# Performance work log

Measured on AMD Instinct MI355X. Metric: run time of the kernel, lower is better.

Reference implementation:

```python
import jax, jax.numpy as jnp
import numpy as np

EMBED_DIM = 768
FF_DIM = 3072
NUM_EXPERTS = 8
TOP_K = 2
CAPACITY_FACTOR = 1.25  # training-mode capacity factor
LB_WEIGHT = 0.01
Z_WEIGHT = 0.001


def setup_inputs() -> dict:
    key = jax.random.key(0)
    k0, k1, k2, k3, k4 = jax.random.split(key, 5)
    B, S, D, F, E = 4, 2048, EMBED_DIM, FF_DIM, NUM_EXPERTS
    scale_d = 1.0 / np.sqrt(D)
    scale_f = 1.0 / np.sqrt(F)
    return {
        "x": jax.random.normal(k0, (B, S, D), dtype=jnp.float32),
        # router gate: nn.Linear(D, E, bias=False) -> weight [E, D]
        "w_gate": jax.random.normal(k1, (E, D), dtype=jnp.float32) * scale_d,
        # stacked expert weights, torch Linear layout [out, in]
        "wi_gate": jax.random.normal(k2, (E, F, D), dtype=jnp.float32) * scale_d,
        "wi_up": jax.random.normal(k3, (E, F, D), dtype=jnp.float32) * scale_d,
        "wo": jax.random.normal(k4, (E, D, F), dtype=jnp.float32) * scale_f,
    }


def moe_forward(x, w_gate, wi_gate, wi_up, wo):
    B, S, D = x.shape
    E = w_gate.shape[0]
    K = TOP_K
    T = B * S
    capacity = max(int(T * K / E * CAPACITY_FACTOR), K)

    xf = x.reshape(T, D)
    router_logits = xf @ w_gate.T                        # [T, E]
    router_probs = jax.nn.softmax(router_logits, axis=-1)
    topk_probs, topk_idx = jax.lax.top_k(router_probs, K)  # [T, K]
    topk_probs = topk_probs / topk_probs.sum(axis=-1, keepdims=True)

    # one-hot dispatch mask [T, K, E]
    onehot = (topk_idx[:, :, None] == jnp.arange(E)[None, None, :]).astype(xf.dtype)
    # per-(k, expert) arrival rank of each token (torch truncates first `capacity`
    # tokens in token-index order, independently per k and per expert)
    rank = ((jnp.cumsum(onehot, axis=0) - onehot) * onehot).sum(-1)  # [T, K]
    keep = (rank < capacity).astype(xf.dtype)                        # [T, K]

    # combine weights per (token, expert) [T, E]
    combine = jnp.einsum('tk,tk,tke->te', topk_probs, keep, onehot)

    out = jnp.zeros_like(xf)
    for e in range(E):  # fixed small structural loop over experts
        gate = jax.nn.silu(xf @ wi_gate[e].T)   # [T, F]
        up = xf @ wi_up[e].T                    # [T, F]
        y = (gate * up) @ wo[e].T               # [T, D]
        out = out + y * combine[:, e:e + 1]

    # auxiliary losses
    expert_mask = onehot.sum(axis=1)            # [T, E]
    f = expert_mask.sum(axis=0) / (T * K)
    P = router_probs.mean(axis=0)
    load_balance_loss = E * (f * P).sum()
    z_loss = jnp.mean(jax.nn.logsumexp(router_logits, axis=-1) ** 2)
    aux_loss = LB_WEIGHT * load_balance_loss + Z_WEIGHT * z_loss

    return out.reshape(B, S, D), aux_loss


def reference(x, w_gate, wi_gate, wi_up, wo):
    return moe_forward(x, w_gate, wi_gate, wi_up, wo)
```

## Files before the change

kernel.cpp:

```cpp
#include <hip/hip_runtime.h>

typedef unsigned short u16;
typedef unsigned int u32;
typedef unsigned long long u64;

#define T_TOK 8192
#define DIM 768
#define FF 3072
#define NE 8
#define CAP 2560
#define LSTR 5120
#define MAXMT 20

typedef __attribute__((ext_vector_type(8))) short s8v;
typedef __attribute__((ext_vector_type(4))) float f4v;

__device__ __forceinline__ u16 f2bf(float f) {
  union { float f; u32 u; } v; v.f = f;
  u32 r = v.u + 0x7FFFu + ((v.u >> 16) & 1u);
  return (u16)(r >> 16);
}

__device__ __forceinline__ void glds16(const void* g, void* l) {
  __builtin_amdgcn_global_load_lds(
      (const __attribute__((address_space(1))) u32*)g,
      (__attribute__((address_space(3))) u32*)l, 16, 0, 0);
}

__global__ void cast_bf16_kernel(const float* __restrict__ src, u16* __restrict__ dst, int n8) {
  int i = blockIdx.x * blockDim.x + threadIdx.x;
  if (i >= n8) return;
  const float4* s4 = (const float4*)src;
  float4 a = s4[2 * i], b = s4[2 * i + 1];
  uint4 o;
  o.x = (u32)f2bf(a.x) | ((u32)f2bf(a.y) << 16);
  o.y = (u32)f2bf(a.z) | ((u32)f2bf(a.w) << 16);
  o.z = (u32)f2bf(b.x) | ((u32)f2bf(b.y) << 16);
  o.w = (u32)f2bf(b.z) | ((u32)f2bf(b.w) << 16);
  ((uint4*)dst)[i] = o;
}

__global__ __launch_bounds__(256) void router_kernel(
    const float* __restrict__ x, const float* __restrict__ wg,
    int* __restrict__ tki, float* __restrict__ tkp,
    float* __restrict__ probs, float* __restrict__ lse2) {
  int lane = threadIdx.x & 63;
  int t = blockIdx.x * 4 + (threadIdx.x >> 6);
  const float* xr = x + (long)t * DIM;
  float acc[NE];
#pragma unroll
  for (int e = 0; e < NE; e++) acc[e] = 0.f;
  for (int i = 0; i < DIM / 64; i++) {
    float xv = xr[lane + 64 * i];
#pragma unroll
    for (int e = 0; e < NE; e++) acc[e] += xv * wg[e * DIM + lane + 64 * i];
  }
#pragma unroll
  for (int off = 32; off > 0; off >>= 1) {
#pragma unroll
    for (int e = 0; e < NE; e++) acc[e] += __shfl_xor(acc[e], off);
  }
  if (lane == 0) {
    float m = acc[0];
#pragma unroll
    for (int e = 1; e < NE; e++) m = fmaxf(m, acc[e]);
    float p[NE], s = 0.f;
#pragma unroll
    for (int e = 0; e < NE; e++) { p[e] = __expf(acc[e] - m); s += p[e]; }
    float inv = 1.f / s;
    int e0 = 0;
#pragma unroll
    for (int e = 1; e < NE; e++) if (acc[e] > acc[e0]) e0 = e;
    int e1 = (e0 == 0) ? 1 : 0;
#pragma unroll
    for (int e = 0; e < NE; e++) if (e != e0 && acc[e] > acc[e1]) e1 = e;
    float p0 = p[e0] * inv, p1 = p[e1] * inv;
    float rn = 1.f / (p0 + p1);
    tki[2 * t] = e0; tki[2 * t + 1] = e1;
    tkp[2 * t] = p0 * rn; tkp[2 * t + 1] = p1 * rn;
    float4 pa = {p[0] * inv, p[1] * inv, p[2] * inv, p[3] * inv};
    float4 pb = {p[4] * inv, p[5] * inv, p[6] * inv, p[7] * inv};
    ((float4*)(probs + t * 8))[0] = pa;
    ((float4*)(probs + t * 8))[1] = pb;
    float lse = __logf(s) + m;
    lse2[t] = lse * lse;
  }
}

__global__ __launch_bounds__(1024) void reduce_router_kernel(
    const int* __restrict__ tki, const float* __restrict__ probs, const float* __restrict__ lse2,
    int* __restrict__ fcnt, float* __restrict__ psum, float* __restrict__ zsum) {
  int t = blockIdx.x * 1024 + threadIdx.x;
  float4 pa = ((const float4*)(probs + t * 8))[0];
  float4 pb = ((const float4*)(probs + t * 8))[1];
  float p[8] = {pa.x, pa.y, pa.z, pa.w, pb.x, pb.y, pb.z, pb.w};
  float z = lse2[t];
  int e0 = tki[2 * t], e1 = tki[2 * t + 1];
  int fc[8];
#pragma unroll
  for (int e = 0; e < 8; e++) fc[e] = (e0 == e ? 1 : 0) + (e1 == e ? 1 : 0);
#pragma unroll
  for (int off = 32; off > 0; off >>= 1) {
#pragma unroll
    for (int e = 0; e < 8; e++) { p[e] += __shfl_xor(p[e], off); fc[e] += __shfl_xor(fc[e], off); }
    z += __shfl_xor(z, off);
  }
  __shared__ float sp[16][9];
  __shared__ int sf[16][8];
  int wv = threadIdx.x >> 6, lane = threadIdx.x & 63;
  if (lane == 0) {
#pragma unroll
    for (int e = 0; e < 8; e++) { sp[wv][e] = p[e]; sf[wv][e] = fc[e]; }
    sp[wv][8] = z;
  }
  __syncthreads();
  if (threadIdx.x < 9) {
    float s = 0.f;
    for (int w = 0; w < 16; w++) s += sp[w][threadIdx.x];
    if (threadIdx.x < 8) atomicAdd(&psum[threadIdx.x], s);
    else atomicAdd(zsum, s);
  }
  if (threadIdx.x >= 64 && threadIdx.x < 72) {
    int e = threadIdx.x - 64;
    int s = 0;
    for (int w = 0; w < 16; w++) s += sf[w][e];
    atomicAdd(&fcnt[e], s);
  }
}

__global__ __launch_bounds__(1024) void rank_dispatch_kernel(
    const int* __restrict__ tki, const float* __restrict__ tkp,
    int* __restrict__ ltk, float* __restrict__ lw,
    int* __restrict__ counts, int* __restrict__ baserow) {
  __shared__ int wave_cnt[2][16][8];
  __shared__ int base[2][8];
  __shared__ int epos[8];
  int tid = threadIdx.x, wv = tid >> 6, lane = tid & 63;
  if (tid < 16) base[tid >> 3][tid & 7] = 0;
  if (tid < 8) epos[tid] = 0;
  __syncthreads();
  u64 lmask = (lane == 63) ? 0x7FFFFFFFFFFFFFFFull : ((1ull << lane) - 1ull);
  for (int c = 0; c < T_TOK / 1024; c++) {
    int t = c * 1024 + tid;
    int e0 = tki[2 * t], e1 = tki[2 * t + 1];
    float p0 = tkp[2 * t], p1 = tkp[2 * t + 1];
    int pre0 = 0, pre1 = 0;
    for (int e = 0; e < 8; e++) {
      u64 m0 = __ballot(e0 == e);
      if (e0 == e) pre0 = __popcll(m0 & lmask);
      if (lane == 0) wave_cnt[0][wv][e] = __popcll(m0);
      u64 m1 = __ballot(e1 == e);
      if (e1 == e) pre1 = __popcll(m1 & lmask);
      if (lane == 0) wave_cnt[1][wv][e] = __popcll(m1);
    }
    __syncthreads();
    if (tid < 16) {
      int k = tid >> 3, e = tid & 7;
      int run = base[k][e];
      for (int w = 0; w < 16; w++) {
        int v = wave_cnt[k][w][e];
        wave_cnt[k][w][e] = run;
        run += v;
      }
      base[k][e] = run;
    }
    __syncthreads();
    int r0 = wave_cnt[0][wv][e0] + pre0;
    int r1 = wave_cnt[1][wv][e1] + pre1;
    if (r0 < CAP) { int p = atomicAdd(&epos[e0], 1); ltk[e0 * LSTR + p] = (t << 1); lw[e0 * LSTR + p] = p0; }
    if (r1 < CAP) { int p = atomicAdd(&epos[e1], 1); ltk[e1 * LSTR + p] = (t << 1) | 1; lw[e1 * LSTR + p] = p1; }
    __syncthreads();
  }
  if (tid == 0) {
    int run = 0;
    for (int e = 0; e < 8; e++) { counts[e] = epos[e]; baserow[e] = run; run += epos[e]; }
  }
}

__global__ __launch_bounds__(256, 2) void gemm1_kernel(
    const u16* __restrict__ xb, const u16* __restrict__ wgb, const u16* __restrict__ wub,
    u16* __restrict__ H, const int* __restrict__ counts, const int* __restrict__ baserow,
    const int* __restrict__ ltk) {
  int id = blockIdx.x;
  int xcd = id & 7;
  int q = id >> 3;
  int gg = q / MAXMT;
  int mt = q - gg * MAXMT;
  int g = gg * 8 + xcd;
  int e = g / 48;
  int nt = g - e * 48;
  int cnt = counts[e];
  if (mt * 128 >= cnt) return;

  __shared__ u16 As[128 * 64];
  __shared__ u16 Bg[64 * 64];
  __shared__ u16 Bu[64 * 64];
  __shared__ int toks[128];
  int tid = threadIdx.x;
  if (tid < 128) {
    int r = mt * 128 + tid; if (r > cnt - 1) r = cnt - 1;
    toks[tid] = ltk[e * LSTR + r] >> 1;
  }
  __syncthreads();
  int rq8 = tid >> 3;
  int swz = ((tid & 7) ^ (rq8 & 7)) * 8;
  long tA0 = toks[rq8], tA1 = toks[32 + rq8], tA2 = toks[64 + rq8], tA3 = toks[96 + rq8];
  const u16* gA0 = xb + tA0 * DIM + swz;
  const u16* gA1 = xb + tA1 * DIM + swz;
  const u16* gA2 = xb + tA2 * DIM + swz;
  const u16* gA3 = xb + tA3 * DIM + swz;
  long bO0 = ((long)e * FF + nt * 64 + rq8) * DIM + swz;
  long bO1 = bO0 + 32l * DIM;
  const u16* gG0 = wgb + bO0; const u16* gG1 = wgb + bO1;
  const u16* gU0 = wub + bO0; const u16* gU1 = wub + bO1;
  u16* dA0 = As + tid * 8; u16* dA1 = dA0 + 2048; u16* dA2 = dA0 + 4096; u16* dA3 = dA0 + 6144;
  u16* dG0 = Bg + tid * 8; u16* dG1 = dG0 + 2048;
  u16* dU0 = Bu + tid * 8; u16* dU1 = dU0 + 2048;

  int lane = tid & 63, wv = tid >> 6;
  int wm = (wv & 1) * 64, wn = (wv >> 1) * 32;
  int lrow = lane & 15, quad = lane >> 4;
  int sl0 = (quad ^ (lrow & 7)) * 8;
  int sl1 = ((quad + 4) ^ (lrow & 7)) * 8;

  f4v zero = {0.f, 0.f, 0.f, 0.f};
  f4v accg[4][2], accu[4][2];
#pragma unroll
  for (int i = 0; i < 4; i++)
#pragma unroll
    for (int j = 0; j < 2; j++) { accg[i][j] = zero; accu[i][j] = zero; }

  for (int kt = 0; kt < DIM / 64; kt++) {
    int ko = kt * 64;
    __syncthreads();
    glds16(gA0 + ko, dA0); glds16(gA1 + ko, dA1);
    glds16(gA2 + ko, dA2); glds16(gA3 + ko, dA3);
    glds16(gG0 + ko, dG0); glds16(gG1 + ko, dG1);
    glds16(gU0 + ko, dU0); glds16(gU1 + ko, dU1);
    __syncthreads();
#pragma unroll
    for (int kk = 0; kk < 2; kk++) {
      int sl = kk ? sl1 : sl0;
      s8v a[4], bgf[2], buf[2];
#pragma unroll
      for (int i = 0; i < 4; i++)
        a[i] = *(const s8v*)&As[(wm + i * 16 + lrow) * 64 + sl];
#pragma unroll
      for (int j = 0; j < 2; j++) {
        bgf[j] = *(const s8v*)&Bg[(wn + j * 16 + lrow) * 64 + sl];
        buf[j] = *(const s8v*)&Bu[(wn + j * 16 + lrow) * 64 + sl];
      }
#pragma unroll
      for (int i = 0; i < 4; i++)
#pragma unroll
        for (int j = 0; j < 2; j++) {
          accg[i][j] = __builtin_amdgcn_mfma_f32_16x16x32_bf16(a[i], bgf[j], accg[i][j], 0, 0, 0);
          accu[i][j] = __builtin_amdgcn_mfma_f32_16x16x32_bf16(a[i], buf[j], accu[i][j], 0, 0, 0);
        }
    }
  }
  long hb = (long)baserow[e] + (long)mt * 128;
#pragma unroll
  for (int i = 0; i < 4; i++) {
#pragma unroll
    for (int r = 0; r < 4; r++) {
      int m = wm + i * 16 + quad * 4 + r;
      if (mt * 128 + m < cnt) {
#pragma unroll
        for (int j = 0; j < 2; j++) {
          float gv = accg[i][j][r], uv = accu[i][j][r];
          float h = gv / (1.f + __expf(-gv)) * uv;
          H[(hb + m) * FF + nt * 64 + wn + j * 16 + lrow] = f2bf(h);
        }
      }
    }
  }
}

__global__ __launch_bounds__(256, 2) void gemm2_kernel(
    const u16* __restrict__ H, const u16* __restrict__ wob,
    float* __restrict__ out, const int* __restrict__ counts, const int* __restrict__ baserow,
    const int* __restrict__ ltk, const float* __restrict__ lw) {
  int id = blockIdx.x;
  int xcd = id & 7;
  int q = id >> 3;
  int gg = q / 6;
  int nt = q - gg * 6;
  int g = gg * 8 + xcd;
  int e = g / MAXMT;
  int mt = g - e * MAXMT;
  int cnt = counts[e];
  if (mt * 128 >= cnt) return;

  __shared__ u16 As[128 * 64];
  __shared__ u16 Bs[128 * 64];
  __shared__ int stok[128];
  __shared__ float sw[128];
  int tid = threadIdx.x;
  if (tid < 128) {
    int r = mt * 128 + tid; if (r > cnt - 1) r = cnt - 1;
    stok[tid] = ltk[e * LSTR + r];
    sw[tid] = lw[e * LSTR + r];
  }
  long hb = (long)baserow[e] + (long)mt * 128;
  int rq8 = tid >> 3;
  int swz = ((tid & 7) ^ (rq8 & 7)) * 8;
  const u16* gA0 = H + (hb + rq8) * FF + swz;
  const u16* gA1 = gA0 + 32l * FF;
  const u16* gA2 = gA0 + 64l * FF;
  const u16* gA3 = gA0 + 96l * FF;
  long bOff = ((long)e * DIM + nt * 128 + rq8) * FF + swz;
  const u16* gB0 = wob + bOff;
  const u16* gB1 = gB0 + 32l * FF;
  const u16* gB2 = gB0 + 64l * FF;
  const u16* gB3 = gB0 + 96l * FF;
  u16* dA0 = As + tid * 8; u16* dA1 = dA0 + 2048; u16* dA2 = dA0 + 4096; u16* dA3 = dA0 + 6144;
  u16* dB0 = Bs + tid * 8; u16* dB1 = dB0 + 2048; u16* dB2 = dB0 + 4096; u16* dB3 = dB0 + 6144;
  int lane = tid & 63, wv = tid >> 6;
  int wm = (wv & 1) * 64, wn = (wv >> 1) * 64;
  int lrow = lane & 15, quad = lane >> 4;
  int sl0 = (quad ^ (lrow & 7)) * 8;
  int sl1 = ((quad + 4) ^ (lrow & 7)) * 8;
  f4v zero = {0.f, 0.f, 0.f, 0.f};
  f4v acc[4][4];
#pragma unroll
  for (int i = 0; i < 4; i++)
#pragma unroll
    for (int j = 0; j < 4; j++) acc[i][j] = zero;

  for (int kt = 0; kt < FF / 64; kt++) {
    int ko = kt * 64;
    __syncthreads();
    glds16(gA0 + ko, dA0); glds16(gA1 + ko, dA1);
    glds16(gA2 + ko, dA2); glds16(gA3 + ko, dA3);
    glds16(gB0 + ko, dB0); glds16(gB1 + ko, dB1);
    glds16(gB2 + ko, dB2); glds16(gB3 + ko, dB3);
    __syncthreads();
#pragma unroll
    for (int kk = 0; kk < 2; kk++) {
      int sl = kk ? sl1 : sl0;
      s8v a[4], b[4];
#pragma unroll
      for (int i = 0; i < 4; i++)
        a[i] = *(const s8v*)&As[(wm + i * 16 + lrow) * 64 + sl];
#pragma unroll
      for (int j = 0; j < 4; j++)
        b[j] = *(const s8v*)&Bs[(wn + j * 16 + lrow) * 64 + sl];
#pragma unroll
      for (int i = 0; i < 4; i++)
#pragma unroll
        for (int j = 0; j < 4; j++)
          acc[i][j] = __builtin_amdgcn_mfma_f32_16x16x32_bf16(a[i], b[j], acc[i][j], 0, 0, 0);
    }
  }
#pragma unroll
  for (int i = 0; i < 4; i++) {
#pragma unroll
    for (int r = 0; r < 4; r++) {
      int m = wm + i * 16 + quad * 4 + r;
      if (mt * 128 + m < cnt) {
        int entry = stok[m];
        int t = entry >> 1;
        float w = sw[m];
        long ob = (long)t * DIM + nt * 128;
#pragma unroll
        for (int j = 0; j < 4; j++)
          atomicAdd(&out[ob + wn + j * 16 + lrow], acc[i][j][r] * w);
      }
    }
  }
}

__global__ void aux_kernel(const int* __restrict__ fcnt, const float* __restrict__ psum,
                           const float* __restrict__ zsum, float* __restrict__ outaux) {
  if (threadIdx.x == 0 && blockIdx.x == 0) {
    float lb = 0.f;
    for (int e = 0; e < 8; e++)
      lb += ((float)fcnt[e] / (float)(T_TOK * 2)) * (psum[e] / (float)T_TOK);
    lb *= 8.f;
    float z = zsum[0] / (float)T_TOK;
    outaux[0] = 0.01f * lb + 0.001f * z;
  }
}

extern "C" void kernel_launch(void* const* d_in, const int* in_sizes, int n_in,
                              void* d_out, int out_size, void* d_ws, size_t ws_size,
                              hipStream_t stream) {
  const float* x = (const float*)d_in[0];
  const float* wgate = (const float*)d_in[1];
  const float* wig = (const float*)d_in[2];
  const float* wiu = (const float*)d_in[3];
  const float* wo = (const float*)d_in[4];
  float* out = (float*)d_out;

  char* ws = (char*)d_ws;
  size_t off = 0;
  auto alloc = [&](size_t bytes) {
    void* p = ws + off;
    off += (bytes + 255) & ~(size_t)255;
    return p;
  };
  int* ctrl = (int*)alloc(256);
  u16* xb = (u16*)alloc((size_t)T_TOK * DIM * 2);
  u16* wgb = (u16*)alloc((size_t)NE * FF * DIM * 2);
  u16* wub = (u16*)alloc((size_t)NE * FF * DIM * 2);
  u16* wob = (u16*)alloc((size_t)NE * DIM * FF * 2);
  u16* Hbuf = (u16*)alloc((size_t)(T_TOK * 2 + 128) * FF * 2);
  int* tki = (int*)alloc((size_t)T_TOK * 2 * 4);
  float* tkp = (float*)alloc((size_t)T_TOK * 2 * 4);
  int* ltk = (int*)alloc((size_t)NE * LSTR * 4);
  float* lw = (float*)alloc((size_t)NE * LSTR * 4);
  float* probs = (float*)alloc((size_t)T_TOK * 8 * 4);
  float* lse2 = (float*)alloc((size_t)T_TOK * 4);

  int* fcnt = ctrl;
  int* counts = ctrl + 8;
  int* baserow = ctrl + 16;
  float* psum = (float*)(ctrl + 24);
  float* zsum = (float*)(ctrl + 32);

  hipMemsetAsync(ctrl, 0, 256, stream);
  hipMemsetAsync(out, 0, (size_t)out_size * 4, stream);
  cast_bf16_kernel<<<T_TOK * DIM / 8 / 256, 256, 0, stream>>>(x, xb, T_TOK * DIM / 8);
  cast_bf16_kernel<<<NE * FF * DIM / 8 / 256, 256, 0, stream>>>(wig, wgb, NE * FF * DIM / 8);
  cast_bf16_kernel<<<NE * FF * DIM / 8 / 256, 256, 0, stream>>>(wiu, wub, NE * FF * DIM / 8);
  cast_bf16_kernel<<<NE * DIM * FF / 8 / 256, 256, 0, stream>>>(wo, wob, NE * DIM * FF / 8);
  router_kernel<<<T_TOK / 4, 256, 0, stream>>>(x, wgate, tki, tkp, probs, lse2);
  reduce_router_kernel<<<T_TOK / 1024, 1024, 0, stream>>>(tki, probs, lse2, fcnt, psum, zsum);
  rank_dispatch_kernel<<<1, 1024, 0, stream>>>(tki, tkp, ltk, lw, counts, baserow);
  gemm1_kernel<<<8 * 48 * MAXMT, 256, 0, stream>>>(xb, wgb, wub, Hbuf, counts, baserow, ltk);
  gemm2_kernel<<<8 * MAXMT * 6, 256, 0, stream>>>(Hbuf, wob, out, counts, baserow, ltk, lw);
  aux_kernel<<<1, 64, 0, stream>>>(fcnt, psum, zsum, out + (size_t)T_TOK * DIM);
}
```

Baseline: 601.7 us.

## Replace atomic scatter with deterministic per-slot buffer and combine kernel; fuse casts

The three weight casts are merged into one launch, and the x-to-bf16 cast is folded into the router kernel. The rank dispatch now places entries at deterministic slots: the k=0 list comes first and the k=1 list is offset by the per-expert k=0 count, which removes the shared-memory atomics. gemm2 writes weighted results into a per-(token,k) fp32 buffer instead of doing atomicAdd into the output, and a new combine kernel sums the two slots per token. This also drops the output memset. The cost is an extra pass over a T*2*D fp32 buffer, which reuses the workspace of the gate weights after gemm1 has finished with them.

```diff
diff --git a/kernel.cpp b/kernel.cpp
--- a/kernel.cpp
+++ b/kernel.cpp
@@ -27,31 +27,38 @@
       (__attribute__((address_space(3))) u32*)l, 16, 0, 0);
 }
 
-__global__ void cast_bf16_kernel(const float* __restrict__ src, u16* __restrict__ dst, int n8) {
-  int i = blockIdx.x * blockDim.x + threadIdx.x;
-  if (i >= n8) return;
-  const float4* s4 = (const float4*)src;
-  float4 a = s4[2 * i], b = s4[2 * i + 1];
+__global__ __launch_bounds__(256) void cast3_kernel(
+    const float* __restrict__ s0, const float* __restrict__ s1, const float* __restrict__ s2,
+    u16* __restrict__ d0, u16* __restrict__ d1, u16* __restrict__ d2, int n8each) {
+  int i = blockIdx.x * 256 + threadIdx.x;
+  const float* s; u16* d; int j;
+  if (i < n8each) { s = s0; d = d0; j = i; }
+  else if (i < 2 * n8each) { s = s1; d = d1; j = i - n8each; }
+  else { s = s2; d = d2; j = i - 2 * n8each; }
+  const float4* s4 = (const float4*)s;
+  float4 a = s4[2 * j], b = s4[2 * j + 1];
   uint4 o;
   o.x = (u32)f2bf(a.x) | ((u32)f2bf(a.y) << 16);
   o.y = (u32)f2bf(a.z) | ((u32)f2bf(a.w) << 16);
   o.z = (u32)f2bf(b.x) | ((u32)f2bf(b.y) << 16);
   o.w = (u32)f2bf(b.z) | ((u32)f2bf(b.w) << 16);
-  ((uint4*)dst)[i] = o;
+  ((uint4*)d)[j] = o;
 }
 
 __global__ __launch_bounds__(256) void router_kernel(
-    const float* __restrict__ x, const float* __restrict__ wg,
+    const float* __restrict__ x, const float* __restrict__ wg, u16* __restrict__ xb,
     int* __restrict__ tki, float* __restrict__ tkp,
     float* __restrict__ probs, float* __restrict__ lse2) {
   int lane = threadIdx.x & 63;
   int t = blockIdx.x * 4 + (threadIdx.x >> 6);
   const float* xr = x + (long)t * DIM;
+  u16* xw = xb + (long)t * DIM;
   float acc[NE];
 #pragma unroll
   for (int e = 0; e < NE; e++) acc[e] = 0.f;
   for (int i = 0; i < DIM / 64; i++) {
     float xv = xr[lane + 64 * i];
+    xw[lane + 64 * i] = f2bf(xv);
 #pragma unroll
     for (int e = 0; e < NE; e++) acc[e] += xv * wg[e * DIM + lane + 64 * i];
   }
@@ -131,13 +138,33 @@
 __global__ __launch_bounds__(1024) void rank_dispatch_kernel(
     const int* __restrict__ tki, const float* __restrict__ tkp,
     int* __restrict__ ltk, float* __restrict__ lw,
-    int* __restrict__ counts, int* __restrict__ baserow) {
+    int* __restrict__ counts, int* __restrict__ baserow, int* __restrict__ kflags) {
   __shared__ int wave_cnt[2][16][8];
   __shared__ int base[2][8];
-  __shared__ int epos[8];
+  __shared__ int sc0[8];
   int tid = threadIdx.x, wv = tid >> 6, lane = tid & 63;
+  int c0w[8];
+#pragma unroll
+  for (int e = 0; e < 8; e++) c0w[e] = 0;
+  for (int c = 0; c < T_TOK / 1024; c++) {
+    int e0 = tki[2 * (c * 1024 + tid)];
+#pragma unroll
+    for (int e = 0; e < 8; e++) {
+      u64 m = __ballot(e0 == e);
+      if (lane == 0) c0w[e] += __popcll(m);
+    }
+  }
+  if (lane == 0) {
+#pragma unroll
+    for (int e = 0; e < 8; e++) wave_cnt[0][wv][e] = c0w[e];
+  }
   if (tid < 16) base[tid >> 3][tid & 7] = 0;
-  if (tid < 8) epos[tid] = 0;
+  __syncthreads();
+  if (tid < 8) {
+    int s = 0;
+    for (int w = 0; w < 16; w++) s += wave_cnt[0][w][tid];
+    sc0[tid] = (s < CAP) ? s : CAP;
+  }
   __syncthreads();
   u64 lmask = (lane == 63) ? 0x7FFFFFFFFFFFFFFFull : ((1ull << lane) - 1ull);
   for (int c = 0; c < T_TOK / 1024; c++) {
@@ -167,13 +194,21 @@
     __syncthreads();
     int r0 = wave_cnt[0][wv][e0] + pre0;
     int r1 = wave_cnt[1][wv][e1] + pre1;
-    if (r0 < CAP) { int p = atomicAdd(&epos[e0], 1); ltk[e0 * LSTR + p] = (t << 1); lw[e0 * LSTR + p] = p0; }
-    if (r1 < CAP) { int p = atomicAdd(&epos[e1], 1); ltk[e1 * LSTR + p] = (t << 1) | 1; lw[e1 * LSTR + p] = p1; }
+    if (r0 < CAP) { ltk[e0 * LSTR + r0] = (t << 1); lw[e0 * LSTR + r0] = p0; }
+    if (r1 < CAP) {
+      int p = sc0[e1] + r1;
+      ltk[e1 * LSTR + p] = (t << 1) | 1; lw[e1 * LSTR + p] = p1;
+    }
+    kflags[t] = (r0 < CAP ? 1 : 0) | (r1 < CAP ? 2 : 0);
     __syncthreads();
   }
   if (tid == 0) {
     int run = 0;
-    for (int e = 0; e < 8; e++) { counts[e] = epos[e]; baserow[e] = run; run += epos[e]; }
+    for (int e = 0; e < 8; e++) {
+      int c1 = base[1][e]; if (c1 > CAP) c1 = CAP;
+      int cnt = sc0[e] + c1;
+      counts[e] = cnt; baserow[e] = run; run += cnt;
+    }
   }
 }
 
@@ -279,7 +314,7 @@
 
 __global__ __launch_bounds__(256, 2) void gemm2_kernel(
     const u16* __restrict__ H, const u16* __restrict__ wob,
-    float* __restrict__ out, const int* __restrict__ counts, const int* __restrict__ baserow,
+    float* __restrict__ ybuf, const int* __restrict__ counts, const int* __restrict__ baserow,
     const int* __restrict__ ltk, const float* __restrict__ lw) {
   int id = blockIdx.x;
   int xcd = id & 7;
@@ -360,15 +395,32 @@
       int m = wm + i * 16 + quad * 4 + r;
       if (mt * 128 + m < cnt) {
         int entry = stok[m];
-        int t = entry >> 1;
         float w = sw[m];
-        long ob = (long)t * DIM + nt * 128;
+        long ob = (long)entry * DIM + nt * 128;
 #pragma unroll
         for (int j = 0; j < 4; j++)
-          atomicAdd(&out[ob + wn + j * 16 + lrow], acc[i][j][r] * w);
+          ybuf[ob + wn + j * 16 + lrow] = acc[i][j][r] * w;
       }
     }
   }
+}
+
+__global__ __launch_bounds__(256) void combine_kernel(
+    const float* __restrict__ ybuf, const int* __restrict__ kflags, float* __restrict__ out) {
+  int idx = blockIdx.x * 256 + threadIdx.x;
+  int t = idx / (DIM / 4);
+  int d4 = idx - t * (DIM / 4);
+  int kf = kflags[t];
+  float4 r = {0.f, 0.f, 0.f, 0.f};
+  if (kf & 1) {
+    float4 a = ((const float4*)(ybuf + (long)(2 * t) * DIM))[d4];
+    r.x += a.x; r.y += a.y; r.z += a.z; r.w += a.w;
+  }
+  if (kf & 2) {
+    float4 b = ((const float4*)(ybuf + (long)(2 * t + 1) * DIM))[d4];
+    r.x += b.x; r.y += b.y; r.z += b.z; r.w += b.w;
+  }
+  ((float4*)out)[idx] = r;
 }
 
 __global__ void aux_kernel(const int* __restrict__ fcnt, const float* __restrict__ psum,
@@ -412,6 +464,8 @@
   float* lw = (float*)alloc((size_t)NE * LSTR * 4);
   float* probs = (float*)alloc((size_t)T_TOK * 8 * 4);
   float* lse2 = (float*)alloc((size_t)T_TOK * 4);
+  int* kflags = (int*)alloc((size_t)T_TOK * 4);
+  float* ybuf = (float*)wgb;
 
   int* fcnt = ctrl;
   int* counts = ctrl + 8;
@@ -419,16 +473,14 @@
   float* psum = (float*)(ctrl + 24);
   float* zsum = (float*)(ctrl + 32);
 
+  const int n8each = NE * FF * DIM / 8;
   hipMemsetAsync(ctrl, 0, 256, stream);
-  hipMemsetAsync(out, 0, (size_t)out_size * 4, stream);
-  cast_bf16_kernel<<<T_TOK * DIM / 8 / 256, 256, 0, stream>>>(x, xb, T_TOK * DIM / 8);
-  cast_bf16_kernel<<<NE * FF * DIM / 8 / 256, 256, 0, stream>>>(wig, wgb, NE * FF * DIM / 8);
-  cast_bf16_kernel<<<NE * FF * DIM / 8 / 256, 256, 0, stream>>>(wiu, wub, NE * FF * DIM / 8);
-  cast_bf16_kernel<<<NE * DIM * FF / 8 / 256, 256, 0, stream>>>(wo, wob, NE * DIM * FF / 8);
-  router_kernel<<<T_TOK / 4, 256, 0, stream>>>(x, wgate, tki, tkp, probs, lse2);
+  cast3_kernel<<<3 * n8each / 256, 256, 0, stream>>>(wig, wiu, wo, wgb, wub, wob, n8each);
+  router_kernel<<<T_TOK / 4, 256, 0, stream>>>(x, wgate, xb, tki, tkp, probs, lse2);
   reduce_router_kernel<<<T_TOK / 1024, 1024, 0, stream>>>(tki, probs, lse2, fcnt, psum, zsum);
-  rank_dispatch_kernel<<<1, 1024, 0, stream>>>(tki, tkp, ltk, lw, counts, baserow);
+  rank_dispatch_kernel<<<1, 1024, 0, stream>>>(tki, tkp, ltk, lw, counts, baserow, kflags);
   gemm1_kernel<<<8 * 48 * MAXMT, 256, 0, stream>>>(xb, wgb, wub, Hbuf, counts, baserow, ltk);
-  gemm2_kernel<<<8 * MAXMT * 6, 256, 0, stream>>>(Hbuf, wob, out, counts, baserow, ltk, lw);
+  gemm2_kernel<<<8 * MAXMT * 6, 256, 0, stream>>>(Hbuf, wob, ybuf, counts, baserow, ltk, lw);
+  combine_kernel<<<T_TOK * DIM / 4 / 256, 256, 0, stream>>>(ybuf, kflags, out);
   aux_kernel<<<1, 64, 0, stream>>>(fcnt, psum, zsum, out + (size_t)T_TOK * DIM);
 }
```

Measured after the change: 582.7 us. 3.2% less time.
